# Performance work log

Hardware: AMD Instinct MI355X
Metric: run time of the kernel (lower is better)

## Reference

```python
import jax, jax.numpy as jnp
import numpy as np

WIN = (16, 9, 9)
WIN_SIZE = WIN[0] * WIN[1] * WIN[2]  # 1296
EPS = float(np.e ** -15)             # ~3.06e-7, matches np.power(np.e, -15)


def setup_inputs() -> dict:
    key = jax.random.key(0)
    k1, k2 = jax.random.split(key)
    shape = (2, 1, 96, 192, 192)  # [B, 1, D, H, W]
    I = jax.random.normal(k1, shape, dtype=jnp.float32)
    J = jax.random.normal(k2, shape, dtype=jnp.float32)
    return {"I": I, "J": J}


def _box_sums(tmp):
    # Grouped conv3d with an all-ones [5,1,16,9,9] kernel: per-channel sliding
    k = jnp.ones((5, 1) + WIN, dtype=tmp.dtype)
    return jax.lax.conv_general_dilated(
        tmp, k,
        window_strides=(1, 1, 1),
        padding=[(0, 0), (WIN[1] // 2, WIN[1] // 2), (WIN[2] // 2, WIN[2] // 2)],
        feature_group_count=5,
        dimension_numbers=("NCDHW", "OIDHW", "NCDHW"),
    )


def reference(I, J):
    # I, J: [B, 1, D, H, W]
    tmp = jnp.concatenate([I, J, I * I, J * J, I * J], axis=1)  # [B,5,D,H,W]
    sums = _box_sums(tmp)  # [B, 5, D-15, H, W]
    I_sum, J_sum = sums[:, 0], sums[:, 1]
    I2_sum, J2_sum, IJ_sum = sums[:, 2], sums[:, 3], sums[:, 4]

    u_I = I_sum / WIN_SIZE
    u_J = J_sum / WIN_SIZE

    cross = IJ_sum - u_J * I_sum - u_I * J_sum + u_I * u_J * WIN_SIZE
    I_var = I2_sum - 2.0 * u_I * I_sum + u_I * u_I * WIN_SIZE
    J_var = J2_sum - 2.0 * u_J * J_sum + u_J * u_J * WIN_SIZE

    nz = (I_var * J_var) > EPS  # bool_non_zero; where false, substitute 1.0
    cross = jnp.where(nz, cross, 1.0)
    I_var = jnp.where(nz, I_var, 1.0)
    J_var = jnp.where(nz, J_var, 1.0)

    cc = cross * cross / (I_var * J_var + EPS)  # [B, D-15, H, W]
    loss = -1.0 * jnp.mean(cc, axis=(1, 2, 3)) + 1.0  # [B]
    return loss, cc
```

## Files before the change

### kernel.cpp

```cpp
#include <hip/hip_runtime.h>


constexpr int N = 2, D = 96, H = 192, W = 192;
constexpr int OD = 81;
constexpr int KD = 16;
constexpr int HWp = H * W;
constexpr float INV_WIN = 1.0f / 1296.0f;
constexpr float EPS_NZ = 3.0590232050182579e-07f;
constexpr int CH = 24;
constexpr int ODPB = 14;

__device__ __forceinline__ unsigned bf16rne(float f) {
  unsigned u = __float_as_uint(f);
  return (u + 0x7fffu + ((u >> 16) & 1u)) >> 16;
}
__device__ __forceinline__ float bf16tof(unsigned h) {
  return __uint_as_float(h << 16);
}

__global__ __launch_bounds__(256)
void k_dw(const float* __restrict__ I, const float* __restrict__ J,
          unsigned* __restrict__ ws, int od0, int c, int odcStride) {
  const int h = blockIdx.x;
  const int n = blockIdx.z;
  const int os = od0 + blockIdx.y * ODPB;
  int oe = od0 + c; if (os + ODPB < oe) oe = os + ODPB;
  if (os >= oe) return;

  const int lane = threadIdx.x & 63;
  const int tile = threadIdx.x >> 6;
  const int wcol = tile * 56 + lane - 4;
  const bool colOK = (wcol >= 0) && (wcol < W);
  const bool stOK  = (lane >= 4) && (lane < 60) && (wcol < W);

  __shared__ float4 x4[4][64]; __shared__ float x1[4][64];
  __shared__ float4 a4[4][64]; __shared__ float a1[4][64];

  const size_t colBase = ((size_t)n * D * H + h) * (size_t)W + wcol;
  const float* Ip = I + colBase;
  const float* Jp = J + colBase;
  unsigned* wbase = ws + ((size_t)n * odcStride * HWp + (size_t)h * W + wcol) * 3;

  const int lm1 = (lane - 1) & 63, lp1 = (lane + 1) & 63;
  const int lm3 = (lane - 3) & 63, lp3 = (lane + 3) & 63;

  float sI = 0.f, sJ = 0.f, sII = 0.f, sJJ = 0.f, sIJ = 0.f;
  for (int d = os; d < os + KD - 1; ++d) {
    const float iv = colOK ? Ip[(size_t)d * HWp] : 0.f;
    const float jv = colOK ? Jp[(size_t)d * HWp] : 0.f;
    sI += iv; sJ += jv;
    sII += iv * iv; sJJ += jv * jv; sIJ += iv * jv;
  }

  float eI = colOK ? Ip[(size_t)(os + KD - 1) * HWp] : 0.f;
  float eJ = colOK ? Jp[(size_t)(os + KD - 1) * HWp] : 0.f;
  float lI = colOK ? Ip[(size_t)os * HWp] : 0.f;
  float lJ = colOK ? Jp[(size_t)os * HWp] : 0.f;

  for (int od = os; od < oe; ++od) {
    const float ceI = eI, ceJ = eJ, clI = lI, clJ = lJ;
    const int odn = od + 1;
    if (odn < oe) {
      eI = colOK ? Ip[(size_t)(odn + KD - 1) * HWp] : 0.f;
      eJ = colOK ? Jp[(size_t)(odn + KD - 1) * HWp] : 0.f;
      lI = colOK ? Ip[(size_t)odn * HWp] : 0.f;
      lJ = colOK ? Jp[(size_t)odn * HWp] : 0.f;
    }
    sI += ceI; sJ += ceJ;
    sII += ceI * ceI; sJJ += ceJ * ceJ; sIJ += ceI * ceJ;
    const float cI = sI, cJ = sJ, cII = sII, cJJ = sJJ, cIJ = sIJ;
    x4[tile][lane] = make_float4(cI, cJ, cII, cJJ); x1[tile][lane] = cIJ;
    sI -= clI; sJ -= clJ;
    sII -= clI * clI; sJJ -= clJ * clJ; sIJ -= clI * clJ;

    const float4 m0 = x4[tile][lm1], m2 = x4[tile][lp1];
    const float  p0 = x1[tile][lm1], p2 = x1[tile][lp1];
    const float aI  = m0.x + cI  + m2.x;
    const float aJ  = m0.y + cJ  + m2.y;
    const float aII = m0.z + cII + m2.z;
    const float aJJ = m0.w + cJJ + m2.w;
    const float aIJ = p0   + cIJ + p2;
    a4[tile][lane] = make_float4(aI, aJ, aII, aJJ); a1[tile][lane] = aIJ;

    const float4 b0 = a4[tile][lm3], b2 = a4[tile][lp3];
    const float  q0 = a1[tile][lm3], q2 = a1[tile][lp3];
    const float r0 = b0.x + aI  + b2.x;
    const float r1 = b0.y + aJ  + b2.y;
    const float r2 = b0.z + aII + b2.z;
    const float r3 = b0.w + aJJ + b2.w;
    const float r4 = q0   + aIJ + q2;

    if (stOK) {
      unsigned* o = wbase + (size_t)(od - od0) * HWp * 3;
      o[0] = bf16rne(r0) | (bf16rne(r1) << 16);
      o[1] = bf16rne(r2) | (bf16rne(r3) << 16);
      o[2] = bf16rne(r4);
    }
  }
}

__global__ __launch_bounds__(192)
void k_hcc(const unsigned* __restrict__ ws, float* __restrict__ cc,
           float* __restrict__ acc, int od0, int odcStride) {
  const int odi = blockIdx.x;
  const int od = od0 + odi;
  const int h0 = blockIdx.y * CH;
  const int n = blockIdx.z;
  const int w = threadIdx.x;
  const unsigned* base =
      ws + ((size_t)n * odcStride * HWp + (size_t)odi * HWp + w) * 3;
  float* ccp = cc + ((size_t)n * OD + od) * (size_t)HWp + w;

  float s0 = 0.f, s1 = 0.f, s2 = 0.f, s3 = 0.f, s4 = 0.f;
  float lsum = 0.f;
  uint3 hist[8];
  const uint3 z3 = make_uint3(0u, 0u, 0u);

  uint3 vN = z3;
  {
    const int hin = h0 - 4;
    if (hin >= 0) vN = *(const uint3*)(base + (size_t)hin * W * 3);
  }
#pragma unroll
  for (int t = 0; t < CH + 8; ++t) {
    const uint3 v = vN;
    if (t + 1 < CH + 8) {
      const int hn = h0 - 4 + t + 1;
      vN = (hn >= 0 && hn < H) ? *(const uint3*)(base + (size_t)hn * W * 3) : z3;
    }
    s0 += bf16tof(v.x & 0xffffu); s1 += bf16tof(v.x >> 16);
    s2 += bf16tof(v.y & 0xffffu); s3 += bf16tof(v.y >> 16);
    s4 += bf16tof(v.z & 0xffffu);
    if (t >= 8) {
      const int h = h0 + t - 8;
      const float cross = s4 - s0 * s1 * INV_WIN;
      const float vI = s2 - s0 * s0 * INV_WIN;
      const float vJ = s3 - s1 * s1 * INV_WIN;
      const float prod = vI * vJ;
      const float c = (prod > EPS_NZ) ? (cross * cross) / (prod + EPS_NZ)
                                      : 1.0f / (1.0f + EPS_NZ);
      ccp[(size_t)h * W] = c;
      lsum += c;
      const uint3 q = hist[t & 7];
      s0 -= bf16tof(q.x & 0xffffu); s1 -= bf16tof(q.x >> 16);
      s2 -= bf16tof(q.y & 0xffffu); s3 -= bf16tof(q.y >> 16);
      s4 -= bf16tof(q.z & 0xffffu);
    }
    hist[t & 7] = v;
  }
  __shared__ float red[3];
#pragma unroll
  for (int off = 32; off > 0; off >>= 1) lsum += __shfl_xor(lsum, off, 64);
  if ((threadIdx.x & 63) == 0) red[threadIdx.x >> 6] = lsum;
  __syncthreads();
  if (threadIdx.x == 0)
    atomicAdd(acc + n * 32 + (odi & 31), red[0] + red[1] + red[2]);
}

__global__ void k_fin(const float* __restrict__ acc, float* __restrict__ out) {
  const int t = threadIdx.x;
  float v = acc[t];
#pragma unroll
  for (int off = 16; off > 0; off >>= 1) v += __shfl_xor(v, off, 32);
  if (t == 0)  out[0] = 1.0f - v * (1.0f / 2985984.0f);
  if (t == 32) out[1] = 1.0f - v * (1.0f / 2985984.0f);
}

extern "C" void kernel_launch(void* const* d_in, const int* in_sizes, int n_in,
                              void* d_out, int out_size, void* d_ws,
                              size_t ws_size, hipStream_t stream) {
  const float* I = (const float*)d_in[0];
  const float* J = (const float*)d_in[1];
  float* out = (float*)d_out;
  float* acc = (float*)d_ws;
  unsigned* planes = (unsigned*)((char*)d_ws + 256);

  hipMemsetAsync(d_ws, 0, 64 * sizeof(float), stream);

  const size_t perOdPerN = (size_t)HWp * 12;
  size_t avail = (ws_size > 256) ? (ws_size - 256) : 0;
  long long odcMax = (long long)(avail / (2 * perOdPerN));
  if (odcMax < 1) odcMax = 1;
  if (odcMax > OD) odcMax = OD;
  const int odc = (int)odcMax;

  float* ccOut = out + 2;
  for (int od0 = 0; od0 < OD; od0 += odc) {
    const int c = (odc < OD - od0) ? odc : (OD - od0);
    const int S = (c + ODPB - 1) / ODPB;
    hipLaunchKernelGGL(k_dw, dim3(H, S, N), dim3(256), 0, stream,
                       I, J, planes, od0, c, odc);
    hipLaunchKernelGGL(k_hcc, dim3(c, H / CH, N), dim3(192), 0, stream,
                       planes, ccOut, acc, od0, odc);
  }
  hipLaunchKernelGGL(k_fin, dim3(1), dim3(64), 0, stream, acc, out);
}
```

Before: 67.87 us.

## Restructure depth/width pass: two columns per thread, full-row shared tiles, no halo waste

The depth-plus-W-box kernel now gives each thread two adjacent columns loaded as float2 and covers a full 192-wide row per 96 threads, two rows per block. This removes the overlapping 64-lane tiles and the lanes that only loaded halo data. It also vectorises the bf16 plane stores, and ODPB is halved to give more blocks. In exchange it needs block-wide barriers for the shared-memory W stencil, plus extra edge-fixup threads for the 9-wide sum near the borders.

```diff
diff --git a/kernel.cpp b/kernel.cpp
--- a/kernel.cpp
+++ b/kernel.cpp
@@ -5,10 +5,11 @@
 constexpr int OD = 81;
 constexpr int KD = 16;
 constexpr int HWp = H * W;
+constexpr int HW2 = HWp / 2;
 constexpr float INV_WIN = 1.0f / 1296.0f;
 constexpr float EPS_NZ = 3.0590232050182579e-07f;
 constexpr int CH = 24;
-constexpr int ODPB = 14;
+constexpr int ODPB = 7;
 
 __device__ __forceinline__ unsigned bf16rne(float f) {
   unsigned u = __float_as_uint(f);
@@ -18,84 +19,118 @@
   return __uint_as_float(h << 16);
 }
 
-__global__ __launch_bounds__(256)
+__global__ __launch_bounds__(192)
 void k_dw(const float* __restrict__ I, const float* __restrict__ J,
           unsigned* __restrict__ ws, int od0, int c, int odcStride) {
-  const int h = blockIdx.x;
-  const int n = blockIdx.z;
+  const int r  = threadIdx.x / 96;
+  const int w2 = threadIdx.x % 96;
+  const int h  = 2 * blockIdx.x + r;
+  const int n  = blockIdx.z;
   const int os = od0 + blockIdx.y * ODPB;
   int oe = od0 + c; if (os + ODPB < oe) oe = os + ODPB;
   if (os >= oe) return;
 
-  const int lane = threadIdx.x & 63;
-  const int tile = threadIdx.x >> 6;
-  const int wcol = tile * 56 + lane - 4;
-  const bool colOK = (wcol >= 0) && (wcol < W);
-  const bool stOK  = (lane >= 4) && (lane < 60) && (wcol < W);
-
-  __shared__ float4 x4[4][64]; __shared__ float x1[4][64];
-  __shared__ float4 a4[4][64]; __shared__ float a1[4][64];
-
-  const size_t colBase = ((size_t)n * D * H + h) * (size_t)W + wcol;
-  const float* Ip = I + colBase;
-  const float* Jp = J + colBase;
-  unsigned* wbase = ws + ((size_t)n * odcStride * HWp + (size_t)h * W + wcol) * 3;
-
-  const int lm1 = (lane - 1) & 63, lp1 = (lane + 1) & 63;
-  const int lm3 = (lane - 3) & 63, lp3 = (lane + 3) & 63;
-
-  float sI = 0.f, sJ = 0.f, sII = 0.f, sJJ = 0.f, sIJ = 0.f;
+  __shared__ float4 x4[2][W + 8]; __shared__ float x1[2][W + 8];
+  __shared__ float4 a4[2][W + 8]; __shared__ float a1[2][W + 8];
+
+  if (threadIdx.x < 8) {
+    const int pos = (threadIdx.x < 4) ? threadIdx.x : (192 + threadIdx.x);
+    x4[0][pos] = make_float4(0.f,0.f,0.f,0.f); x1[0][pos] = 0.f;
+    x4[1][pos] = make_float4(0.f,0.f,0.f,0.f); x1[1][pos] = 0.f;
+  }
+  __syncthreads();
+
+  const int c0 = 2 * w2;
+  const int p0 = 4 + c0;
+  const size_t colBase = ((size_t)n * D * H + h) * (size_t)W + c0;
+  const float2* Ip = (const float2*)(I + colBase);
+  const float2* Jp = (const float2*)(J + colBase);
+  unsigned* wbase = ws + ((size_t)n * odcStride * HWp + (size_t)h * W + c0) * 3;
+
+  int pe = -1;
+  if (w2 < 3) pe = w2 + 1;
+  else if (w2 >= 93) pe = w2 + 103;
+
+  float2 sI = {0.f,0.f}, sJ = {0.f,0.f}, sII = {0.f,0.f},
+         sJJ = {0.f,0.f}, sIJ = {0.f,0.f};
   for (int d = os; d < os + KD - 1; ++d) {
-    const float iv = colOK ? Ip[(size_t)d * HWp] : 0.f;
-    const float jv = colOK ? Jp[(size_t)d * HWp] : 0.f;
-    sI += iv; sJ += jv;
-    sII += iv * iv; sJJ += jv * jv; sIJ += iv * jv;
-  }
-
-  float eI = colOK ? Ip[(size_t)(os + KD - 1) * HWp] : 0.f;
-  float eJ = colOK ? Jp[(size_t)(os + KD - 1) * HWp] : 0.f;
-  float lI = colOK ? Ip[(size_t)os * HWp] : 0.f;
-  float lJ = colOK ? Jp[(size_t)os * HWp] : 0.f;
+    const float2 iv = Ip[(size_t)d * HW2];
+    const float2 jv = Jp[(size_t)d * HW2];
+    sI.x += iv.x; sI.y += iv.y; sJ.x += jv.x; sJ.y += jv.y;
+    sII.x += iv.x*iv.x; sII.y += iv.y*iv.y;
+    sJJ.x += jv.x*jv.x; sJJ.y += jv.y*jv.y;
+    sIJ.x += iv.x*jv.x; sIJ.y += iv.y*jv.y;
+  }
+
+  float2 eI = Ip[(size_t)(os + KD - 1) * HW2];
+  float2 eJ = Jp[(size_t)(os + KD - 1) * HW2];
+  float2 lI = Ip[(size_t)os * HW2];
+  float2 lJ = Jp[(size_t)os * HW2];
 
   for (int od = os; od < oe; ++od) {
-    const float ceI = eI, ceJ = eJ, clI = lI, clJ = lJ;
+    const float2 ceI = eI, ceJ = eJ, clI = lI, clJ = lJ;
     const int odn = od + 1;
     if (odn < oe) {
-      eI = colOK ? Ip[(size_t)(odn + KD - 1) * HWp] : 0.f;
-      eJ = colOK ? Jp[(size_t)(odn + KD - 1) * HWp] : 0.f;
-      lI = colOK ? Ip[(size_t)odn * HWp] : 0.f;
-      lJ = colOK ? Jp[(size_t)odn * HWp] : 0.f;
-    }
-    sI += ceI; sJ += ceJ;
-    sII += ceI * ceI; sJJ += ceJ * ceJ; sIJ += ceI * ceJ;
-    const float cI = sI, cJ = sJ, cII = sII, cJJ = sJJ, cIJ = sIJ;
-    x4[tile][lane] = make_float4(cI, cJ, cII, cJJ); x1[tile][lane] = cIJ;
-    sI -= clI; sJ -= clJ;
-    sII -= clI * clI; sJJ -= clJ * clJ; sIJ -= clI * clJ;
-
-    const float4 m0 = x4[tile][lm1], m2 = x4[tile][lp1];
-    const float  p0 = x1[tile][lm1], p2 = x1[tile][lp1];
-    const float aI  = m0.x + cI  + m2.x;
-    const float aJ  = m0.y + cJ  + m2.y;
-    const float aII = m0.z + cII + m2.z;
-    const float aJJ = m0.w + cJJ + m2.w;
-    const float aIJ = p0   + cIJ + p2;
-    a4[tile][lane] = make_float4(aI, aJ, aII, aJJ); a1[tile][lane] = aIJ;
-
-    const float4 b0 = a4[tile][lm3], b2 = a4[tile][lp3];
-    const float  q0 = a1[tile][lm3], q2 = a1[tile][lp3];
-    const float r0 = b0.x + aI  + b2.x;
-    const float r1 = b0.y + aJ  + b2.y;
-    const float r2 = b0.z + aII + b2.z;
-    const float r3 = b0.w + aJJ + b2.w;
-    const float r4 = q0   + aIJ + q2;
-
-    if (stOK) {
-      unsigned* o = wbase + (size_t)(od - od0) * HWp * 3;
-      o[0] = bf16rne(r0) | (bf16rne(r1) << 16);
-      o[1] = bf16rne(r2) | (bf16rne(r3) << 16);
-      o[2] = bf16rne(r4);
-    }
+      eI = Ip[(size_t)(odn + KD - 1) * HW2];
+      eJ = Jp[(size_t)(odn + KD - 1) * HW2];
+      lI = Ip[(size_t)odn * HW2];
+      lJ = Jp[(size_t)odn * HW2];
+    }
+    sI.x += ceI.x; sI.y += ceI.y; sJ.x += ceJ.x; sJ.y += ceJ.y;
+    sII.x += ceI.x*ceI.x; sII.y += ceI.y*ceI.y;
+    sJJ.x += ceJ.x*ceJ.x; sJJ.y += ceJ.y*ceJ.y;
+    sIJ.x += ceI.x*ceJ.x; sIJ.y += ceI.y*ceJ.y;
+    const float4 xc0 = make_float4(sI.x, sJ.x, sII.x, sJJ.x);
+    const float4 xc1 = make_float4(sI.y, sJ.y, sII.y, sJJ.y);
+    const float  xe0 = sIJ.x, xe1 = sIJ.y;
+    x4[r][p0] = xc0;     x1[r][p0] = xe0;
+    x4[r][p0+1] = xc1;   x1[r][p0+1] = xe1;
+    sI.x -= clI.x; sI.y -= clI.y; sJ.x -= clJ.x; sJ.y -= clJ.y;
+    sII.x -= clI.x*clI.x; sII.y -= clI.y*clI.y;
+    sJJ.x -= clJ.x*clJ.x; sJJ.y -= clJ.y*clJ.y;
+    sIJ.x -= clI.x*clJ.x; sIJ.y -= clI.y*clJ.y;
+
+    asm volatile("s_waitcnt lgkmcnt(0)" ::: "memory");
+    __builtin_amdgcn_s_barrier();
+    const float4 xm = x4[r][p0 - 1]; const float xme = x1[r][p0 - 1];
+    const float4 xp = x4[r][p0 + 2]; const float xpe = x1[r][p0 + 2];
+    const float4 aC0 = make_float4(xm.x + xc0.x + xc1.x, xm.y + xc0.y + xc1.y,
+                                   xm.z + xc0.z + xc1.z, xm.w + xc0.w + xc1.w);
+    const float  aE0 = xme + xe0 + xe1;
+    const float4 aC1 = make_float4(xc0.x + xc1.x + xp.x, xc0.y + xc1.y + xp.y,
+                                   xc0.z + xc1.z + xp.z, xc0.w + xc1.w + xp.w);
+    const float  aE1 = xe0 + xe1 + xpe;
+    a4[r][p0] = aC0;     a1[r][p0] = aE0;
+    a4[r][p0+1] = aC1;   a1[r][p0+1] = aE1;
+    if (pe >= 0) {
+      const float4 e0 = x4[r][pe - 1], e1 = x4[r][pe], e2 = x4[r][pe + 1];
+      a4[r][pe] = make_float4(e0.x + e1.x + e2.x, e0.y + e1.y + e2.y,
+                              e0.z + e1.z + e2.z, e0.w + e1.w + e2.w);
+      a1[r][pe] = x1[r][pe - 1] + x1[r][pe] + x1[r][pe + 1];
+    }
+    asm volatile("s_waitcnt lgkmcnt(0)" ::: "memory");
+    __builtin_amdgcn_s_barrier();
+    const float4 bm3 = a4[r][p0 - 3]; const float em3 = a1[r][p0 - 3];
+    const float4 bp3 = a4[r][p0 + 3]; const float ep3 = a1[r][p0 + 3];
+    const float4 bm2 = a4[r][p0 - 2]; const float em2 = a1[r][p0 - 2];
+    const float4 bp4 = a4[r][p0 + 4]; const float ep4 = a1[r][p0 + 4];
+    const float r0 = bm3.x + aC0.x + bp3.x;
+    const float r1 = bm3.y + aC0.y + bp3.y;
+    const float r2 = bm3.z + aC0.z + bp3.z;
+    const float r3 = bm3.w + aC0.w + bp3.w;
+    const float r4 = em3 + aE0 + ep3;
+    const float q0 = bm2.x + aC1.x + bp4.x;
+    const float q1 = bm2.y + aC1.y + bp4.y;
+    const float q2 = bm2.z + aC1.z + bp4.z;
+    const float q3 = bm2.w + aC1.w + bp4.w;
+    const float q4 = em2 + aE1 + ep4;
+    unsigned* o = wbase + (size_t)(od - od0) * HWp * 3;
+    *(uint2*)(o)     = make_uint2(bf16rne(r0) | (bf16rne(r1) << 16),
+                                  bf16rne(r2) | (bf16rne(r3) << 16));
+    *(uint2*)(o + 2) = make_uint2(bf16rne(r4),
+                                  bf16rne(q0) | (bf16rne(q1) << 16));
+    *(uint2*)(o + 4) = make_uint2(bf16rne(q2) | (bf16rne(q3) << 16),
+                                  bf16rne(q4));
   }
 }
 
@@ -188,7 +223,7 @@
   for (int od0 = 0; od0 < OD; od0 += odc) {
     const int c = (odc < OD - od0) ? odc : (OD - od0);
     const int S = (c + ODPB - 1) / ODPB;
-    hipLaunchKernelGGL(k_dw, dim3(H, S, N), dim3(256), 0, stream,
+    hipLaunchKernelGGL(k_dw, dim3(H / 2, S, N), dim3(192), 0, stream,
                        I, J, planes, od0, c, odc);
     hipLaunchKernelGGL(k_hcc, dim3(c, H / CH, N), dim3(192), 0, stream,
                        planes, ccOut, acc, od0, odc);
```

Result: slower. 71.31 us (+5.1%).
